# Optimization experiments

Measured on AMD Instinct MI355X. Metric: run time of the kernel, lower is better.

Reference implementation:

```python
import jax, jax.numpy as jnp
import numpy as np
import math

TAU = 2.0
V_THRESHOLD = 1.0
ALPHA = 5.0  # surrogate-gradient sharpness


@jax.custom_vjp
def spike(x):
    # Heaviside step: 1.0 where x > 0 else 0.0
    return (x > 0).astype(x.dtype)


def _spike_fwd(x):
    return spike(x), x


def _spike_bwd(x, g):
    # SurrGradSpike backward: alpha/2 / (1 + (pi/2 * alpha * x)^2) * g
    scaled = (math.pi / 2.0) * ALPHA * x
    return ((ALPHA / 2.0) / (1.0 + scaled * scaled) * g,)


spike.defvjp(_spike_fwd, _spike_bwd)


def setup_inputs() -> dict:
    key = jax.random.key(0)
    T, B, N = 100, 256, 2048
    inputs = jax.random.normal(key, (T, B, N), dtype=jnp.float32)
    return {"inputs": inputs}


def reference(inputs) -> jnp.ndarray:
    # LIF neuron recurrence with synaptic current delayed by one step.
    # inputs: [T, B, N]; output spikes: [T, B, N]
    T, B, N = inputs.shape
    decay = 1.0 - 1.0 / TAU

    def step(carry, h1):
        mem, syn = carry
        mthr = mem - V_THRESHOLD
        out = spike(mthr)
        rst = jax.lax.stop_gradient(out)  # detach_reset=True
        new_mem = (decay * mem + syn) * (1.0 - rst)
        return (new_mem, h1), out

    init = (jnp.zeros((B, N), dtype=inputs.dtype),
            jnp.zeros((B, N), dtype=inputs.dtype))
    _, spk = jax.lax.scan(step, init, inputs)
    return spk  # [T, B, N], matches torch stack(dim=1).permute(1,0,2)
```

## Files before the change

kernel.cpp:

```cpp
#include <hip/hip_runtime.h>


constexpr int T_STEPS = 100;
constexpr int PF = 4;

typedef float v2f __attribute__((ext_vector_type(2)));

__global__ __launch_bounds__(256) void lif_kernel(const v2f* __restrict__ in,
                                                  v2f* __restrict__ out,
                                                  int bn2) {
    const int i = blockIdx.x * blockDim.x + threadIdx.x;

    const v2f* __restrict__ ip = in + i;
    v2f* __restrict__ op = out + i;

    v2f mem = 0.0f;
    v2f syn = 0.0f;

    v2f hP[PF];
#pragma unroll
    for (int k = 0; k < PF; ++k) {
        hP[k] = __builtin_nontemporal_load(ip + (long)k * bn2);
    }

#pragma unroll
    for (int t = 0; t < T_STEPS; ++t) {
        v2f hn = 0.0f;
        if (t + PF < T_STEPS) {
            hn = __builtin_nontemporal_load(ip + (long)(t + PF) * bn2);
        }

        v2f o;
        o.x = mem.x > 1.0f ? 1.0f : 0.0f;
        o.y = mem.y > 1.0f ? 1.0f : 0.0f;

        __builtin_nontemporal_store(o, op + (long)t * bn2);

        mem.x = (o.x != 0.0f) ? 0.0f : fmaf(0.5f, mem.x, syn.x);
        mem.y = (o.y != 0.0f) ? 0.0f : fmaf(0.5f, mem.y, syn.y);

        const int idx = t % PF;
        syn = hP[idx];
        hP[idx] = hn;

        __syncthreads();
    }
}

extern "C" void kernel_launch(void* const* d_in, const int* in_sizes, int n_in,
                              void* d_out, int out_size, void* d_ws, size_t ws_size,
                              hipStream_t stream) {
    const float* in = (const float*)d_in[0];
    float* out = (float*)d_out;

    const int total = in_sizes[0];
    const int bn = total / T_STEPS;
    const int bn2 = bn / 2;

    const int block = 256;
    const int grid = bn2 / block;

    lif_kernel<<<grid, block, 0, stream>>>((const v2f*)in, (v2f*)out, bn2);
}
```

Before: 330.5 us.

## Process time steps in chunks of ten with double-buffered loads, drop per-step barrier

```diff
diff --git a/kernel.cpp b/kernel.cpp
--- a/kernel.cpp
+++ b/kernel.cpp
@@ -2,7 +2,8 @@
 
 
 constexpr int T_STEPS = 100;
-constexpr int PF = 4;
+constexpr int C = 10;
+constexpr int NCH = T_STEPS / C;
 
 typedef float v2f __attribute__((ext_vector_type(2)));
 
@@ -10,6 +11,7 @@
                                                   v2f* __restrict__ out,
                                                   int bn2) {
     const int i = blockIdx.x * blockDim.x + threadIdx.x;
+    if (i >= bn2) return;
 
     const v2f* __restrict__ ip = in + i;
     v2f* __restrict__ op = out + i;
@@ -17,33 +19,42 @@
     v2f mem = 0.0f;
     v2f syn = 0.0f;
 
-    v2f hP[PF];
+    v2f h[C];
+    v2f hn[C];
+    v2f o[C];
+
 #pragma unroll
-    for (int k = 0; k < PF; ++k) {
-        hP[k] = __builtin_nontemporal_load(ip + (long)k * bn2);
+    for (int k = 0; k < C; ++k) {
+        h[k] = __builtin_nontemporal_load(ip + (long)k * bn2);
     }
 
 #pragma unroll
-    for (int t = 0; t < T_STEPS; ++t) {
-        v2f hn = 0.0f;
-        if (t + PF < T_STEPS) {
-            hn = __builtin_nontemporal_load(ip + (long)(t + PF) * bn2);
+    for (int c = 0; c < NCH; ++c) {
+        if (c + 1 < NCH) {
+#pragma unroll
+            for (int k = 0; k < C; ++k) {
+                hn[k] = __builtin_nontemporal_load(ip + (long)((c + 1) * C + k) * bn2);
+            }
         }
 
-        v2f o;
-        o.x = mem.x > 1.0f ? 1.0f : 0.0f;
-        o.y = mem.y > 1.0f ? 1.0f : 0.0f;
+#pragma unroll
+        for (int k = 0; k < C; ++k) {
+            o[k].x = mem.x > 1.0f ? 1.0f : 0.0f;
+            o[k].y = mem.y > 1.0f ? 1.0f : 0.0f;
+            mem.x = (o[k].x != 0.0f) ? 0.0f : fmaf(0.5f, mem.x, syn.x);
+            mem.y = (o[k].y != 0.0f) ? 0.0f : fmaf(0.5f, mem.y, syn.y);
+            syn = h[k];
+        }
 
-        __builtin_nontemporal_store(o, op + (long)t * bn2);
+#pragma unroll
+        for (int k = 0; k < C; ++k) {
+            __builtin_nontemporal_store(o[k], op + (long)(c * C + k) * bn2);
+        }
 
-        mem.x = (o.x != 0.0f) ? 0.0f : fmaf(0.5f, mem.x, syn.x);
-        mem.y = (o.y != 0.0f) ? 0.0f : fmaf(0.5f, mem.y, syn.y);
-
-        const int idx = t % PF;
-        syn = hP[idx];
-        hP[idx] = hn;
-
-        __syncthreads();
+#pragma unroll
+        for (int k = 0; k < C; ++k) {
+            h[k] = hn[k];
+        }
     }
 }
 
```

Measured after the change: 326.7 us. No clear change (-1.1%).
